# Kernel tuning notes

Measured on AMD Instinct MI355X. Metric: run time of the kernel, lower is better.

Reference implementation:

```python
import jax, jax.numpy as jnp
import numpy as np

N = 200_000        # atoms
E = 800_000        # directed edges (pairs e, e^1 are mutual reverses)
H = 512            # hidden_size
AF = 133           # atom_feat_size
BF = 14            # bond_feat_size
B = 4096           # num graphs


def setup_inputs() -> dict:
    key = jax.random.key(0)
    ks = jax.random.split(key, 8)
    atom_hiddens = jax.random.normal(ks[0], (N, H), dtype=jnp.float32)
    # undirected bonds, then interleave as (src,dst),(dst,src) so rev[e] = e ^ 1
    src = jax.random.randint(ks[1], (E // 2,), 0, N, dtype=jnp.int32)
    dst = jax.random.randint(ks[2], (E // 2,), 0, N, dtype=jnp.int32)
    heads = jnp.stack([src, dst], axis=1).reshape(-1)   # [E]
    tails = jnp.stack([dst, src], axis=1).reshape(-1)   # [E]
    edge_index = jnp.stack([heads, tails], axis=0)      # [2, E]
    rev_edge_index = jnp.arange(E, dtype=jnp.int32) ^ 1
    batch = jnp.sort(jax.random.randint(ks[3], (N,), 0, B, dtype=jnp.int32))
    batch = batch.at[-1].set(B - 1)  # batch[-1]+1 == B, matching the torch code
    s = 1.0 / np.sqrt(H)
    return {
        "atom_hiddens": atom_hiddens,
        "W_node": jax.random.normal(ks[4], (H, AF), dtype=jnp.float32) * s,
        "b_node": jnp.zeros((AF,), dtype=jnp.float32),
        "W_edge": jax.random.normal(ks[5], (H, BF), dtype=jnp.float32) * s,
        "b_edge": jnp.zeros((BF,), dtype=jnp.float32),
        "W_g1": jax.random.normal(ks[6], (H, H), dtype=jnp.float32) * s,
        "b_g1": jnp.zeros((H,), dtype=jnp.float32),
        "W_g2": jax.random.normal(ks[7], (H, 1), dtype=jnp.float32) * s,
        "b_g2": jnp.zeros((1,), dtype=jnp.float32),
        "edge_index": edge_index,
        "rev_edge_index": rev_edge_index,
        "batch": batch,
        "num_graphs": B,
    }


def reference(atom_hiddens, W_node, b_node, W_edge, b_edge, W_g1, b_g1,
              W_g2, b_g2, edge_index, rev_edge_index, batch, num_graphs):
    # graph pooling: index_add_ over the sorted batch vector
    graph_emb = jax.ops.segment_sum(atom_hiddens, batch, num_segments=num_graphs)
    # node head
    node_pred = atom_hiddens @ W_node + b_node
    # edge dedup: the torch loop keeps edge e iff its reverse was not yet
    # visited, i.e. iff e < rev_edge_index[e] (rev is an involution), giving
    # exactly E//2 kept edges.
    e_ids = jnp.arange(edge_index.shape[1])
    keep = jnp.nonzero(e_ids < rev_edge_index, size=edge_index.shape[1] // 2,
                       fill_value=0)[0]
    a1 = edge_index[0, keep]
    a2 = edge_index[1, keep]
    bond_emb = 0.5 * (atom_hiddens[a1] + atom_hiddens[a2])  # [E//2, H]
    edge_pred = bond_emb @ W_edge + b_edge
    # graph head: Linear -> ReLU -> Linear
    graph_pred = jax.nn.relu(graph_emb @ W_g1 + b_g1) @ W_g2 + b_g2
    return node_pred, edge_pred, graph_pred
```

## Files before the change

kernel.cpp:

```cpp
#include <hip/hip_runtime.h>

#define NATOMS 200000
#define NEDGE  800000
#define NBOND  400000
#define HDIM   512
#define AF     133
#define BFEAT  14
#define NGRAPH 4096

#define NODE_OUT_SZ (NATOMS * AF)
#define EDGE_OUT_SZ (NBOND * BFEAT)

#define WS_P     0
#define WS_BMAT  12800000
#define WS_BIAS  12963840
#define WS_GEF   12964480
#define WS_WG1T  21353088

typedef _Float16 half8 __attribute__((ext_vector_type(8)));
typedef float floatx4 __attribute__((ext_vector_type(4)));

__global__ void pack_kernel(const float* __restrict__ Wn, const float* __restrict__ bn,
                            const float* __restrict__ We, const float* __restrict__ be,
                            const float* __restrict__ Wg1, const float* __restrict__ bg2,
                            _Float16* __restrict__ Bmat, float* __restrict__ bias,
                            _Float16* __restrict__ Wg1t, float* __restrict__ gpred) {
    int idx = blockIdx.x * 256 + threadIdx.x;
    if (idx < 160 * 512) {
        int n = idx >> 9, k = idx & 511;
        float v = 0.f;
        if (n < AF)              v = Wn[k * AF + n];
        else if (n < AF + BFEAT) v = We[k * BFEAT + (n - AF)];
        Bmat[idx] = (_Float16)v;
    } else if (idx < 160 * 512 + 512 * 512) {
        int i = idx - 160 * 512;
        int n = i >> 9, k = i & 511;
        Wg1t[i] = (_Float16)Wg1[k * HDIM + n];
    } else if (idx < 160 * 512 + 512 * 512 + 160) {
        int n = idx - (160 * 512 + 512 * 512);
        float v = 0.f;
        if (n < AF)              v = bn[n];
        else if (n < AF + BFEAT) v = be[n - AF];
        bias[n] = v;
    } else if (idx < 160 * 512 + 512 * 512 + 160 + NGRAPH) {
        gpred[idx - (160 * 512 + 512 * 512 + 160)] = bg2[0];
    }
}

__global__ void zero_ge(float4* __restrict__ GEf4) {
    GEf4[blockIdx.x * 256 + threadIdx.x] = make_float4(0.f, 0.f, 0.f, 0.f);
}

__global__ __launch_bounds__(256, 3) void gemm_node(const float* __restrict__ A,
                                                    const _Float16* __restrict__ Bm,
                                                    const float* __restrict__ bias,
                                                    const int* __restrict__ batch,
                                                    float* __restrict__ node_out,
                                                    float* __restrict__ P,
                                                    float* __restrict__ GEf) {
    __shared__ _Float16 As[2][128][72];
    __shared__ int bg[128];

    const int t    = threadIdx.x;
    const int bm   = blockIdx.x;
    const int w    = t >> 6, l = t & 63, quad = l >> 4, lr = l & 15;
    const int wm   = w & 1, wn = w >> 1;

    if (t < 128) {
        int grow = bm * 128 + t;
        bg[t] = (grow < NATOMS) ? batch[grow] : -1;
    }

    floatx4 acc[4][5];
#pragma unroll
    for (int mt = 0; mt < 4; ++mt)
#pragma unroll
        for (int nt = 0; nt < 5; ++nt)
            acc[mt][nt] = (floatx4){0.f, 0.f, 0.f, 0.f};

    const int arow0 = t >> 2;
    const int aseg  = (t & 3) * 16;
    const int pc    = t & 63;
    const int pq    = w;

    int boff[5];
#pragma unroll
    for (int nt = 0; nt < 5; ++nt)
        boff[nt] = (wn * 80 + nt * 16 + lr) * HDIM + quad * 8;

    float4 av[2][4];
    auto load_tile = [&](int ko) {
        const int k0 = ko * 64;
#pragma unroll
        for (int p = 0; p < 2; ++p) {
            long grow = (long)bm * 128 + arow0 + p * 64;
            if (grow < NATOMS) {
                const float4* src = (const float4*)(A + grow * HDIM + k0 + aseg);
                av[p][0] = src[0]; av[p][1] = src[1]; av[p][2] = src[2]; av[p][3] = src[3];
            } else {
                av[p][0] = av[p][1] = av[p][2] = av[p][3] = make_float4(0.f, 0.f, 0.f, 0.f);
            }
        }
    };
    auto cvt_store = [&](int buf) {
#pragma unroll
        for (int p = 0; p < 2; ++p) {
            int row = arow0 + p * 64;
            half8 h0 = {(_Float16)av[p][0].x, (_Float16)av[p][0].y, (_Float16)av[p][0].z, (_Float16)av[p][0].w,
                        (_Float16)av[p][1].x, (_Float16)av[p][1].y, (_Float16)av[p][1].z, (_Float16)av[p][1].w};
            half8 h1 = {(_Float16)av[p][2].x, (_Float16)av[p][2].y, (_Float16)av[p][2].z, (_Float16)av[p][2].w,
                        (_Float16)av[p][3].x, (_Float16)av[p][3].y, (_Float16)av[p][3].z, (_Float16)av[p][3].w};
            *(half8*)&As[buf][row][aseg]     = h0;
            *(half8*)&As[buf][row][aseg + 8] = h1;
        }
    };

    load_tile(0);
    cvt_store(0);
    __syncthreads();

    for (int ko = 0; ko < 8; ++ko) {
        const int k0  = ko * 64;
        const int cur = ko & 1;

        half8 bfa[5], bfb[5];
#pragma unroll
        for (int nt = 0; nt < 5; ++nt) bfa[nt] = *(const half8*)(Bm + boff[nt] + k0);
#pragma unroll
        for (int nt = 0; nt < 5; ++nt) bfb[nt] = *(const half8*)(Bm + boff[nt] + k0 + 32);
        if (ko < 7) load_tile(ko + 1);

        {
            half8 af[4];
#pragma unroll
            for (int mt = 0; mt < 4; ++mt)
                af[mt] = *(const half8*)&As[cur][wm * 64 + mt * 16 + lr][quad * 8];
#pragma unroll
            for (int mt = 0; mt < 4; ++mt)
#pragma unroll
                for (int nt = 0; nt < 5; ++nt)
                    acc[mt][nt] = __builtin_amdgcn_mfma_f32_16x16x32_f16(af[mt], bfa[nt], acc[mt][nt], 0, 0, 0);
#pragma unroll
            for (int mt = 0; mt < 4; ++mt)
                af[mt] = *(const half8*)&As[cur][wm * 64 + mt * 16 + lr][32 + quad * 8];
#pragma unroll
            for (int mt = 0; mt < 4; ++mt)
#pragma unroll
                for (int nt = 0; nt < 5; ++nt)
                    acc[mt][nt] = __builtin_amdgcn_mfma_f32_16x16x32_f16(af[mt], bfb[nt], acc[mt][nt], 0, 0, 0);
        }

        {
            float psum = 0.f;
            int pg = bg[pq * 32];
#pragma unroll
            for (int rb = 0; rb < 32; rb += 8) {
                float vals[8];
#pragma unroll
                for (int i = 0; i < 8; ++i)
                    vals[i] = (float)As[cur][pq * 32 + rb + i][pc];
#pragma unroll
                for (int i = 0; i < 8; ++i) {
                    int r = pq * 32 + rb + i;
                    int gid = bg[r];
                    if (gid != pg) {
                        if (pg >= 0) atomicAdd(&GEf[(size_t)pg * HDIM + k0 + pc], psum);
                        psum = 0.f; pg = gid;
                    }
                    psum += vals[i];
                }
            }
            if (pg >= 0) atomicAdd(&GEf[(size_t)pg * HDIM + k0 + pc], psum);
        }

        if (ko < 7) {
            cvt_store(cur ^ 1);
            __syncthreads();
        }
    }

    float biasv[5];
#pragma unroll
    for (int nt = 0; nt < 5; ++nt) biasv[nt] = bias[wn * 80 + nt * 16 + lr];
#pragma unroll
    for (int mt = 0; mt < 4; ++mt) {
        int rbase = bm * 128 + wm * 64 + mt * 16 + quad * 4;
#pragma unroll
        for (int r = 0; r < 4; ++r) {
            int grow = rbase + r;
            if (grow >= NATOMS) continue;
#pragma unroll
            for (int nt = 0; nt < 5; ++nt) {
                int gcol = wn * 80 + nt * 16 + lr;
                float v = acc[mt][nt][r] + biasv[nt];
                if (gcol < AF)                  node_out[(long)grow * AF + gcol] = v;
                else if (gcol < AF + BFEAT)     P[(long)grow * 16 + (gcol - AF)] = v;
            }
        }
    }
}

__global__ __launch_bounds__(256) void edge_kernel(const int* __restrict__ ei,
                                                   const float* __restrict__ P,
                                                   float* __restrict__ eout) {
    int t  = threadIdx.x;
    int q  = t & 3, bi = t >> 2;
    int b  = blockIdx.x * 64 + bi;
    if (b >= NBOND) return;
    int e  = 2 * b;
    int a1 = ei[e];
    int a2 = ei[NEDGE + e];
    const float4 v1 = *(const float4*)(P + (size_t)a1 * 16 + q * 4);
    const float4 v2 = *(const float4*)(P + (size_t)a2 * 16 + q * 4);
    float r[4] = {0.5f * (v1.x + v2.x), 0.5f * (v1.y + v2.y),
                  0.5f * (v1.z + v2.z), 0.5f * (v1.w + v2.w)};
    float* dst = eout + (size_t)b * BFEAT + q * 4;
    int rem = BFEAT - q * 4;
#pragma unroll
    for (int i = 0; i < 4; ++i)
        if (i < rem) dst[i] = r[i];
}

__global__ __launch_bounds__(256) void gemm_graph(const float* __restrict__ GEf,
                                                  const _Float16* __restrict__ Bt,
                                                  const float* __restrict__ bg1,
                                                  const float* __restrict__ wg2,
                                                  float* __restrict__ gpred) {
    __shared__ _Float16 As[128][72];
    __shared__ _Float16 Bs[128][72];

    const int t   = threadIdx.x;
    const int bmb = blockIdx.x, bnb = blockIdx.y;
    const int w   = t >> 6, l = t & 63, quad = l >> 4, lr = l & 15;
    const int wm  = w & 1, wn = w >> 1;

    floatx4 acc[4][4];
    for (int mt = 0; mt < 4; ++mt)
        for (int nt = 0; nt < 4; ++nt)
            acc[mt][nt] = (floatx4){0.f, 0.f, 0.f, 0.f};

    const int arow0 = t >> 2;
    const int aseg  = (t & 3) * 16;

    for (int ko = 0; ko < 8; ++ko) {
        const int k0 = ko * 64;
        float4 av[2][4];
        for (int p = 0; p < 2; ++p) {
            int row = bmb * 128 + arow0 + p * 64;
            const float4* src = (const float4*)(GEf + (size_t)row * HDIM + k0 + aseg);
            av[p][0] = src[0]; av[p][1] = src[1]; av[p][2] = src[2]; av[p][3] = src[3];
        }
        uint4 bvv[4];
        for (int it = 0; it < 4; ++it) {
            int idx = t + it * 256;
            int row = idx >> 3, c = (idx & 7) * 8;
            bvv[it] = *(const uint4*)(Bt + (size_t)(bnb * 128 + row) * HDIM + k0 + c);
        }
        __syncthreads();
        for (int p = 0; p < 2; ++p) {
            int row = arow0 + p * 64;
            half8 h0 = {(_Float16)av[p][0].x, (_Float16)av[p][0].y, (_Float16)av[p][0].z, (_Float16)av[p][0].w,
                        (_Float16)av[p][1].x, (_Float16)av[p][1].y, (_Float16)av[p][1].z, (_Float16)av[p][1].w};
            half8 h1 = {(_Float16)av[p][2].x, (_Float16)av[p][2].y, (_Float16)av[p][2].z, (_Float16)av[p][2].w,
                        (_Float16)av[p][3].x, (_Float16)av[p][3].y, (_Float16)av[p][3].z, (_Float16)av[p][3].w};
            *(half8*)&As[row][aseg]     = h0;
            *(half8*)&As[row][aseg + 8] = h1;
        }
        for (int it = 0; it < 4; ++it) {
            int idx = t + it * 256;
            int row = idx >> 3, c = (idx & 7) * 8;
            *(uint4*)&Bs[row][c] = bvv[it];
        }
        __syncthreads();
        for (int kk = 0; kk < 64; kk += 32) {
            half8 af[4], bf[4];
            for (int mt = 0; mt < 4; ++mt)
                af[mt] = *(const half8*)&As[wm * 64 + mt * 16 + lr][kk + quad * 8];
            for (int nt = 0; nt < 4; ++nt)
                bf[nt] = *(const half8*)&Bs[wn * 64 + nt * 16 + lr][kk + quad * 8];
            for (int mt = 0; mt < 4; ++mt)
                for (int nt = 0; nt < 4; ++nt)
                    acc[mt][nt] = __builtin_amdgcn_mfma_f32_16x16x32_f16(af[mt], bf[nt], acc[mt][nt], 0, 0, 0);
        }
    }

    float bg1v[4], wg2v[4];
    for (int nt = 0; nt < 4; ++nt) {
        int col = bnb * 128 + wn * 64 + nt * 16 + lr;
        bg1v[nt] = bg1[col];
        wg2v[nt] = wg2[col];
    }
    for (int mt = 0; mt < 4; ++mt) {
        for (int r = 0; r < 4; ++r) {
            int row = bmb * 128 + wm * 64 + mt * 16 + quad * 4 + r;
            float partial = 0.f;
            for (int nt = 0; nt < 4; ++nt) {
                float v = acc[mt][nt][r] + bg1v[nt];
                v = v > 0.f ? v : 0.f;
                partial += v * wg2v[nt];
            }
            partial += __shfl_xor(partial, 1);
            partial += __shfl_xor(partial, 2);
            partial += __shfl_xor(partial, 4);
            partial += __shfl_xor(partial, 8);
            if (lr == 0) atomicAdd(&gpred[row], partial);
        }
    }
}

extern "C" void kernel_launch(void* const* d_in, const int* in_sizes, int n_in,
                              void* d_out, int out_size, void* d_ws, size_t ws_size,
                              hipStream_t stream) {
    const float* A    = (const float*)d_in[0];
    const float* Wn   = (const float*)d_in[1];
    const float* bn   = (const float*)d_in[2];
    const float* We   = (const float*)d_in[3];
    const float* be   = (const float*)d_in[4];
    const float* Wg1  = (const float*)d_in[5];
    const float* bg1  = (const float*)d_in[6];
    const float* Wg2  = (const float*)d_in[7];
    const float* bg2  = (const float*)d_in[8];
    const int*   ei   = (const int*)d_in[9];
    const int*   batch= (const int*)d_in[11];

    char* ws = (char*)d_ws;
    float*    P    = (float*)(ws + WS_P);
    _Float16* Bmat = (_Float16*)(ws + WS_BMAT);
    float*    bias = (float*)(ws + WS_BIAS);
    float*    GEf  = (float*)(ws + WS_GEF);
    _Float16* Wg1t = (_Float16*)(ws + WS_WG1T);

    float* node_out = (float*)d_out;
    float* edge_out = node_out + NODE_OUT_SZ;
    float* gpred    = edge_out + EDGE_OUT_SZ;

    pack_kernel<<<dim3(1361), dim3(256), 0, stream>>>(Wn, bn, We, be, Wg1, bg2, Bmat, bias, Wg1t, gpred);
    zero_ge<<<dim3(NGRAPH * HDIM / 4 / 256), dim3(256), 0, stream>>>((float4*)GEf);
    gemm_node<<<dim3((NATOMS + 127) / 128), dim3(256), 0, stream>>>(A, Bmat, bias, batch, node_out, P, GEf);
    edge_kernel<<<dim3((NBOND + 63) / 64), dim3(256), 0, stream>>>(ei, P, edge_out);
    gemm_graph<<<dim3(32, 4), dim3(256), 0, stream>>>(GEf, Wg1t, bg1, Wg2, gpred);
}
```

Baseline: 801.3 us.

## Stage weight tiles in LDS and coalesce node GEMM epilogue through shared memory

```diff
diff --git a/kernel.cpp b/kernel.cpp
--- a/kernel.cpp
+++ b/kernel.cpp
@@ -51,15 +51,21 @@
     GEf4[blockIdx.x * 256 + threadIdx.x] = make_float4(0.f, 0.f, 0.f, 0.f);
 }
 
-__global__ __launch_bounds__(256, 3) void gemm_node(const float* __restrict__ A,
-                                                    const _Float16* __restrict__ Bm,
-                                                    const float* __restrict__ bias,
-                                                    const int* __restrict__ batch,
-                                                    float* __restrict__ node_out,
-                                                    float* __restrict__ P,
-                                                    float* __restrict__ GEf) {
-    __shared__ _Float16 As[2][128][72];
-    __shared__ int bg[128];
+__global__ __launch_bounds__(256) void gemm_node(const float* __restrict__ A,
+                                                 const _Float16* __restrict__ Bm,
+                                                 const float* __restrict__ bias,
+                                                 const int* __restrict__ batch,
+                                                 float* __restrict__ node_out,
+                                                 float* __restrict__ P,
+                                                 float* __restrict__ GEf) {
+    __shared__ union SMem {
+        struct {
+            _Float16 As[128][72];
+            _Float16 Bs[160][72];
+            int      bg[128];
+        } m;
+        float C[64][164];
+    } sm;
 
     const int t    = threadIdx.x;
     const int bm   = blockIdx.x;
@@ -68,7 +74,7 @@
 
     if (t < 128) {
         int grow = bm * 128 + t;
-        bg[t] = (grow < NATOMS) ? batch[grow] : -1;
+        sm.m.bg[t] = (grow < NATOMS) ? batch[grow] : -1;
     }
 
     floatx4 acc[4][5];
@@ -83,17 +89,13 @@
     const int pc    = t & 63;
     const int pq    = w;
 
-    int boff[5];
-#pragma unroll
-    for (int nt = 0; nt < 5; ++nt)
-        boff[nt] = (wn * 80 + nt * 16 + lr) * HDIM + quad * 8;
-
-    float4 av[2][4];
-    auto load_tile = [&](int ko) {
+    for (int ko = 0; ko < 8; ++ko) {
         const int k0 = ko * 64;
+        float4 av[2][4];
 #pragma unroll
         for (int p = 0; p < 2; ++p) {
-            long grow = (long)bm * 128 + arow0 + p * 64;
+            int row = arow0 + p * 64;
+            long grow = (long)bm * 128 + row;
             if (grow < NATOMS) {
                 const float4* src = (const float4*)(A + grow * HDIM + k0 + aseg);
                 av[p][0] = src[0]; av[p][1] = src[1]; av[p][2] = src[2]; av[p][3] = src[3];
@@ -101,8 +103,14 @@
                 av[p][0] = av[p][1] = av[p][2] = av[p][3] = make_float4(0.f, 0.f, 0.f, 0.f);
             }
         }
-    };
-    auto cvt_store = [&](int buf) {
+        uint4 bv[5];
+#pragma unroll
+        for (int it = 0; it < 5; ++it) {
+            int idx = t + it * 256;
+            int row = idx >> 3, c = (idx & 7) * 8;
+            bv[it] = *(const uint4*)(Bm + row * HDIM + k0 + c);
+        }
+        __syncthreads();
 #pragma unroll
         for (int p = 0; p < 2; ++p) {
             int row = arow0 + p * 64;
@@ -110,59 +118,43 @@
                         (_Float16)av[p][1].x, (_Float16)av[p][1].y, (_Float16)av[p][1].z, (_Float16)av[p][1].w};
             half8 h1 = {(_Float16)av[p][2].x, (_Float16)av[p][2].y, (_Float16)av[p][2].z, (_Float16)av[p][2].w,
                         (_Float16)av[p][3].x, (_Float16)av[p][3].y, (_Float16)av[p][3].z, (_Float16)av[p][3].w};
-            *(half8*)&As[buf][row][aseg]     = h0;
-            *(half8*)&As[buf][row][aseg + 8] = h1;
-        }
-    };
-
-    load_tile(0);
-    cvt_store(0);
-    __syncthreads();
-
-    for (int ko = 0; ko < 8; ++ko) {
-        const int k0  = ko * 64;
-        const int cur = ko & 1;
-
-        half8 bfa[5], bfb[5];
-#pragma unroll
-        for (int nt = 0; nt < 5; ++nt) bfa[nt] = *(const half8*)(Bm + boff[nt] + k0);
-#pragma unroll
-        for (int nt = 0; nt < 5; ++nt) bfb[nt] = *(const half8*)(Bm + boff[nt] + k0 + 32);
-        if (ko < 7) load_tile(ko + 1);
-
-        {
-            half8 af[4];
-#pragma unroll
-            for (int mt = 0; mt < 4; ++mt)
-                af[mt] = *(const half8*)&As[cur][wm * 64 + mt * 16 + lr][quad * 8];
+            *(half8*)&sm.m.As[row][aseg]     = h0;
+            *(half8*)&sm.m.As[row][aseg + 8] = h1;
+        }
+#pragma unroll
+        for (int it = 0; it < 5; ++it) {
+            int idx = t + it * 256;
+            int row = idx >> 3, c = (idx & 7) * 8;
+            *(uint4*)&sm.m.Bs[row][c] = bv[it];
+        }
+        __syncthreads();
+#pragma unroll
+        for (int kk = 0; kk < 64; kk += 32) {
+            half8 af[4], bf[5];
+#pragma unroll
+            for (int mt = 0; mt < 4; ++mt)
+                af[mt] = *(const half8*)&sm.m.As[wm * 64 + mt * 16 + lr][kk + quad * 8];
+#pragma unroll
+            for (int nt = 0; nt < 5; ++nt)
+                bf[nt] = *(const half8*)&sm.m.Bs[wn * 80 + nt * 16 + lr][kk + quad * 8];
 #pragma unroll
             for (int mt = 0; mt < 4; ++mt)
 #pragma unroll
                 for (int nt = 0; nt < 5; ++nt)
-                    acc[mt][nt] = __builtin_amdgcn_mfma_f32_16x16x32_f16(af[mt], bfa[nt], acc[mt][nt], 0, 0, 0);
-#pragma unroll
-            for (int mt = 0; mt < 4; ++mt)
-                af[mt] = *(const half8*)&As[cur][wm * 64 + mt * 16 + lr][32 + quad * 8];
-#pragma unroll
-            for (int mt = 0; mt < 4; ++mt)
-#pragma unroll
-                for (int nt = 0; nt < 5; ++nt)
-                    acc[mt][nt] = __builtin_amdgcn_mfma_f32_16x16x32_f16(af[mt], bfb[nt], acc[mt][nt], 0, 0, 0);
-        }
-
+                    acc[mt][nt] = __builtin_amdgcn_mfma_f32_16x16x32_f16(af[mt], bf[nt], acc[mt][nt], 0, 0, 0);
+        }
         {
             float psum = 0.f;
-            int pg = bg[pq * 32];
+            int pg = sm.m.bg[pq * 32];
 #pragma unroll
             for (int rb = 0; rb < 32; rb += 8) {
                 float vals[8];
 #pragma unroll
                 for (int i = 0; i < 8; ++i)
-                    vals[i] = (float)As[cur][pq * 32 + rb + i][pc];
+                    vals[i] = (float)sm.m.As[pq * 32 + rb + i][pc];
 #pragma unroll
                 for (int i = 0; i < 8; ++i) {
-                    int r = pq * 32 + rb + i;
-                    int gid = bg[r];
+                    int gid = sm.m.bg[pq * 32 + rb + i];
                     if (gid != pg) {
                         if (pg >= 0) atomicAdd(&GEf[(size_t)pg * HDIM + k0 + pc], psum);
                         psum = 0.f; pg = gid;
@@ -172,30 +164,40 @@
             }
             if (pg >= 0) atomicAdd(&GEf[(size_t)pg * HDIM + k0 + pc], psum);
         }
-
-        if (ko < 7) {
-            cvt_store(cur ^ 1);
-            __syncthreads();
-        }
     }
 
     float biasv[5];
 #pragma unroll
     for (int nt = 0; nt < 5; ++nt) biasv[nt] = bias[wn * 80 + nt * 16 + lr];
-#pragma unroll
-    for (int mt = 0; mt < 4; ++mt) {
-        int rbase = bm * 128 + wm * 64 + mt * 16 + quad * 4;
-#pragma unroll
-        for (int r = 0; r < 4; ++r) {
-            int grow = rbase + r;
-            if (grow >= NATOMS) continue;
-#pragma unroll
-            for (int nt = 0; nt < 5; ++nt) {
-                int gcol = wn * 80 + nt * 16 + lr;
-                float v = acc[mt][nt][r] + biasv[nt];
-                if (gcol < AF)                  node_out[(long)grow * AF + gcol] = v;
-                else if (gcol < AF + BFEAT)     P[(long)grow * 16 + (gcol - AF)] = v;
+
+#pragma unroll
+    for (int phase = 0; phase < 2; ++phase) {
+        __syncthreads();
+        if (wm == phase) {
+#pragma unroll
+            for (int mt = 0; mt < 4; ++mt)
+#pragma unroll
+                for (int rr = 0; rr < 4; ++rr) {
+                    int lrow = mt * 16 + quad * 4 + rr;
+#pragma unroll
+                    for (int nt = 0; nt < 5; ++nt)
+                        sm.C[lrow][wn * 80 + nt * 16 + lr] = acc[mt][nt][rr] + biasv[nt];
+                }
+        }
+        __syncthreads();
+        const int gbase = bm * 128 + phase * 64;
+        for (int r16 = 0; r16 < 16; ++r16) {
+            int row  = w * 16 + r16;
+            int grow = gbase + row;
+            if (grow < NATOMS) {
+                for (int c = l; c < AF; c += 64)
+                    node_out[(long)grow * AF + c] = sm.C[row][c];
             }
+        }
+        for (int idx = t; idx < 1024; idx += 256) {
+            int r = idx >> 4, c = idx & 15;
+            int grow = gbase + r;
+            if (grow < NATOMS) P[(size_t)grow * 16 + c] = sm.C[r][AF + c];
         }
     }
 }
```

New measurement: 762.9 us. 4.8% less time.
